# Kernel tuning notes

Hardware: AMD Instinct MI355X
Metric: run time of the kernel (lower is better)

## Reference

```python
import jax, jax.numpy as jnp
import numpy as np

# DeformConv (v1, mmcv-style) config
N, C, H, W = 4, 64, 128, 128
OUT_C, KH, KW = 64, 3, 3
STRIDE, PAD, DIL, DG = 1, 1, 1, 1  # groups = 1


def setup_inputs() -> dict:
    key = jax.random.key(0)
    k1, k2, k3 = jax.random.split(key, 3)
    x = jax.random.normal(k1, (N, C, H, W), dtype=jnp.float32)
    offset = jax.random.normal(k2, (N, 2 * DG * KH * KW, H, W), dtype=jnp.float32)
    n_fan = C * KH * KW
    std = 1.0 / np.sqrt(n_fan)
    weight = jax.random.uniform(k3, (OUT_C, C, KH, KW), minval=-std, maxval=std, dtype=jnp.float32)
    return {"input_tensor": x, "offset": offset, "weight": weight}


def _deform_conv(x, offset, weight, stride, padding, dilation, dg):
    n, c, h, w = x.shape
    o, cin_g, kh, kw = weight.shape
    k = kh * kw
    ho = (h + 2 * padding - dilation * (kh - 1) - 1) // stride + 1
    wo = (w + 2 * padding - dilation * (kw - 1) - 1) // stride + 1

    # offset layout: [n, dg*k*2, ho, wo] with (dy, dx) pairs per kernel point
    off = offset.reshape(n, dg, k, 2, ho, wo)
    dy, dx = off[:, :, :, 0], off[:, :, :, 1]  # [n, dg, k, ho, wo]

    ky, kx = jnp.meshgrid(jnp.arange(kh), jnp.arange(kw), indexing="ij")
    ky = ky.reshape(k).astype(x.dtype)
    kx = kx.reshape(k).astype(x.dtype)

    base_y = (jnp.arange(ho) * stride - padding).astype(x.dtype)
    base_x = (jnp.arange(wo) * stride - padding).astype(x.dtype)
    # sampling positions [n, dg, k, ho, wo]
    py = base_y[None, None, None, :, None] + (ky * dilation)[None, None, :, None, None] + dy
    px = base_x[None, None, None, None, :] + (kx * dilation)[None, None, :, None, None] + dx

    cg = c // dg
    xg = x.reshape(n, dg, cg, h * w)

    y0 = jnp.floor(py)
    x0 = jnp.floor(px)
    ly = py - y0  # bilinear weights
    lx = px - x0
    y0i = y0.astype(jnp.int32)
    x0i = x0.astype(jnp.int32)

    def gather(yi, xi):
        # zero contribution for out-of-bounds neighbors (matches mmcv bilinear)
        valid = (yi >= 0) & (yi < h) & (xi >= 0) & (xi < w)
        idx = jnp.clip(yi, 0, h - 1) * w + jnp.clip(xi, 0, w - 1)  # [n, dg, k, ho, wo]
        v = jnp.take_along_axis(xg, idx.reshape(n, dg, 1, -1), axis=3)  # [n, dg, cg, k*ho*wo]
        v = v.reshape(n, dg, cg, k, ho, wo)
        return v * valid[:, :, None].astype(x.dtype)

    v00 = gather(y0i, x0i)
    v01 = gather(y0i, x0i + 1)
    v10 = gather(y0i + 1, x0i)
    v11 = gather(y0i + 1, x0i + 1)

    wy = ly[:, :, None]  # [n, dg, 1, k, ho, wo]
    wx = lx[:, :, None]
    sampled = (v00 * (1 - wy) * (1 - wx) + v01 * (1 - wy) * wx
               + v10 * wy * (1 - wx) + v11 * wy * wx)
    sampled = sampled.reshape(n, c, k, ho, wo)  # dg*cg == c, groups == 1

    return jnp.einsum("nckhw,ock->nohw", sampled, weight.reshape(o, cin_g, k))


def reference(input_tensor, offset, weight):
    return _deform_conv(input_tensor, offset, weight, STRIDE, PAD, DIL, DG)
```

## Files before the change

### kernel.cpp

```cpp
#include <hip/hip_runtime.h>

#define HW 16384
#define CIN 64
#define COUT 64
#define HH 128
#define WW 128
#define NB 4
#define PXB 16
#define TPB 8

typedef __attribute__((ext_vector_type(8))) short bf16x8;
typedef __attribute__((ext_vector_type(4))) float f32x4;
typedef __attribute__((ext_vector_type(4))) unsigned short u16x4;

__device__ __forceinline__ unsigned short f32_bf16(float f) {
  unsigned u = __builtin_bit_cast(unsigned, f);
  u += 0x7fffu + ((u >> 16) & 1u);
  return (unsigned short)(u >> 16);
}
__device__ __forceinline__ float bits_f32(unsigned u) {
  return __builtin_bit_cast(float, u);
}

#define SYNCB()                                              \
  do {                                                       \
    asm volatile("s_waitcnt lgkmcnt(0)" ::: "memory");       \
    __builtin_amdgcn_s_barrier();                            \
    __builtin_amdgcn_sched_barrier(0);                       \
  } while (0)

__global__ __launch_bounds__(256) void prep_kernel(
    const float* __restrict__ x, const float* __restrict__ w,
    unsigned short* __restrict__ xt, unsigned short* __restrict__ wt) {
  __shared__ float tile[64][65];
  const int bid = blockIdx.x;
  if (bid < 1024) {
    const int n = bid >> 8;
    const int hw0 = (bid & 255) * 64;
    const int tx = threadIdx.x & 63;
    const int ty = threadIdx.x >> 6;
    const float* xp = x + (size_t)n * CIN * HW;
    #pragma unroll
    for (int c = ty; c < 64; c += 4)
      tile[c][tx] = xp[(size_t)c * HW + hw0 + tx];
    __syncthreads();
    unsigned short* xtp = xt + (size_t)n * HW * CIN;
    #pragma unroll
    for (int hw = ty; hw < 64; hw += 4)
      xtp[(size_t)(hw0 + hw) * CIN + tx] = f32_bf16(tile[tx][hw]);
  } else {
    const int i = (bid - 1024) * 256 + threadIdx.x;
    if (i < 64 * 576) {
      const int o = i / 576;
      const int t = i % 576;
      const int c = t & 63;
      const int k = t >> 6;
      wt[i] = f32_bf16(w[((size_t)o * 64 + c) * 9 + k]);
    }
  }
}

__global__ __launch_bounds__(256, 2) void deform_mfma(
    const unsigned short* __restrict__ xt, const float* __restrict__ offset,
    const unsigned short* __restrict__ wt, float* __restrict__ out) {
  __shared__ unsigned short s[PXB][584];
  __shared__ f32x4 pw[2][144];
  __shared__ uint2 pidx[2][144];
  const int tid = threadIdx.x;
  const int wave = tid >> 6;
  const int lane = tid & 63;
  const int g = lane >> 4;
  const int li = lane & 15;
  const int base = blockIdx.x * (PXB * TPB);
  const int n = base >> 14;
  const int rem_base = base & 16383;

  const float* offb = offset + (size_t)n * 18 * HW;
  const unsigned short* xli = xt + (size_t)n * HW * CIN + li * 4;

  const int px0 = tid & 15;
  const int tap0 = tid >> 4;
  const bool pthr = tap0 < 9;
  const int px = wave * 4 + g;

  bf16x8 bv[18];
  {
    const unsigned short* bp = wt + ((size_t)(wave * 16 + li)) * 576 + g * 8;
    #pragma unroll
    for (int i = 0; i < 18; ++i)
      bv[i] = *(const bf16x8*)(bp + i * 32);
  }

  #define PARAMS(tt, wb)                                                   \
    do {                                                                   \
      const int rem = rem_base + (tt) * PXB + px0;                         \
      const int y = rem >> 7;                                              \
      const int x = rem & 127;                                             \
      const float fy = floorf(dy);                                         \
      const float fx = floorf(dx);                                         \
      const float ly = dy - fy;                                            \
      const float lx = dx - fx;                                            \
      const int y0 = y - 1 + (tap0 / 3) + (int)fy;                         \
      const int x0 = x - 1 + (tap0 % 3) + (int)fx;                         \
      const int y1 = y0 + 1, x1 = x0 + 1;                                  \
      const bool vy0 = (unsigned)y0 < (unsigned)HH;                        \
      const bool vy1 = (unsigned)y1 < (unsigned)HH;                        \
      const bool vx0 = (unsigned)x0 < (unsigned)WW;                        \
      const bool vx1 = (unsigned)x1 < (unsigned)WW;                        \
      const int cy0 = min(max(y0, 0), HH - 1);                             \
      const int cy1 = min(max(y1, 0), HH - 1);                             \
      const int cx0 = min(max(x0, 0), WW - 1);                             \
      const int cx1 = min(max(x1, 0), WW - 1);                             \
      const float omly = 1.f - ly, omlx = 1.f - lx;                        \
      f32x4 w4;                                                            \
      w4[0] = (vy0 && vx0) ? omly * omlx : 0.f;                            \
      w4[1] = (vy0 && vx1) ? omly * lx : 0.f;                              \
      w4[2] = (vy1 && vx0) ? ly * omlx : 0.f;                              \
      w4[3] = (vy1 && vx1) ? ly * lx : 0.f;                                \
      const unsigned i00 = (unsigned)(cy0 * WW + cx0);                     \
      const unsigned i01 = (unsigned)(cy0 * WW + cx1);                     \
      const unsigned i10 = (unsigned)(cy1 * WW + cx0);                     \
      const unsigned i11 = (unsigned)(cy1 * WW + cx1);                     \
      pw[wb][tid] = w4;                                                    \
      pidx[wb][tid] = make_uint2(i00 | (i01 << 16), i10 | (i11 << 16));    \
    } while (0)

  u16x4 V00[9], V01[9], V10[9], V11[9];

  #define GATHERS(rb)                                                      \
    do {                                                                   \
      uint2 id[9];                                                         \
      _Pragma("unroll")                                                    \
      for (int k = 0; k < 9; ++k) id[k] = pidx[rb][k * 16 + px];           \
      _Pragma("unroll")                                                    \
      for (int k = 0; k < 9; ++k) {                                        \
        V00[k] = *(const u16x4*)(xli + (size_t)(id[k].x & 0xffffu) * CIN); \
        V01[k] = *(const u16x4*)(xli + (size_t)(id[k].x >> 16) * CIN);     \
        V10[k] = *(const u16x4*)(xli + (size_t)(id[k].y & 0xffffu) * CIN); \
        V11[k] = *(const u16x4*)(xli + (size_t)(id[k].y >> 16) * CIN);     \
      }                                                                    \
      __builtin_amdgcn_sched_barrier(0);                                   \
    } while (0)

  #define MFMA_OUT(remt)                                                   \
    do {                                                                   \
      f32x4 acc0 = {0.f, 0.f, 0.f, 0.f};                                   \
      f32x4 acc1 = {0.f, 0.f, 0.f, 0.f};                                   \
      const unsigned short* ap = &s[li][g * 8];                            \
      _Pragma("unroll")                                                    \
      for (int i = 0; i < 18; i += 2) {                                    \
        bf16x8 av0 = *(const bf16x8*)(ap + i * 32);                        \
        bf16x8 av1 = *(const bf16x8*)(ap + (i + 1) * 32);                  \
        acc0 = __builtin_amdgcn_mfma_f32_16x16x32_bf16(av0, bv[i], acc0, 0, 0, 0); \
        acc1 = __builtin_amdgcn_mfma_f32_16x16x32_bf16(av1, bv[i + 1], acc1, 0, 0, 0); \
      }                                                                    \
      const f32x4 acc = acc0 + acc1;                                       \
      const int oc = wave * 16 + li;                                       \
      float* ob = out + ((size_t)n * COUT + oc) * HW + (remt) + g * 4;     \
      *(f32x4*)ob = acc;                                                   \
    } while (0)

  float dy = 0.f, dx = 0.f;
  if (pthr) {
    const int rem = rem_base + px0;
    dy = offb[(size_t)(2 * tap0) * HW + rem];
    dx = offb[(size_t)(2 * tap0 + 1) * HW + rem];
  }
  if (pthr) PARAMS(0, 0);
  if (pthr) {
    const int rem = rem_base + PXB + px0;
    dy = offb[(size_t)(2 * tap0) * HW + rem];
    dx = offb[(size_t)(2 * tap0 + 1) * HW + rem];
  }
  SYNCB();
  GATHERS(0);

  int prev_rem0 = 0;

  #pragma unroll 1
  for (int t = 0; t < TPB; ++t) {
    const int rem0 = rem_base + t * PXB;

    if (t > 0) MFMA_OUT(prev_rem0);

    if (t + 1 < TPB && pthr) PARAMS(t + 1, (t + 1) & 1);

    if (t + 2 < TPB && pthr) {
      const int rem = rem_base + (t + 2) * PXB + px0;
      dy = offb[(size_t)(2 * tap0) * HW + rem];
      dx = offb[(size_t)(2 * tap0 + 1) * HW + rem];
    }

    SYNCB();

    #pragma unroll
    for (int k = 0; k < 9; ++k) {
      const f32x4 w = pw[t & 1][k * 16 + px];
      float a0 = 0.f, a1 = 0.f, a2 = 0.f, a3 = 0.f;
      #define CORNER(v, wc)                                        \
        a0 = fmaf(bits_f32((unsigned)(v)[0] << 16), (wc), a0);     \
        a1 = fmaf(bits_f32((unsigned)(v)[1] << 16), (wc), a1);     \
        a2 = fmaf(bits_f32((unsigned)(v)[2] << 16), (wc), a2);     \
        a3 = fmaf(bits_f32((unsigned)(v)[3] << 16), (wc), a3);
      CORNER(V00[k], w[0]);
      CORNER(V01[k], w[1]);
      CORNER(V10[k], w[2]);
      CORNER(V11[k], w[3]);
      #undef CORNER
      unsigned r01, r23;
      asm("v_cvt_pk_bf16_f32 %0, %1, %2" : "=v"(r01) : "v"(a0), "v"(a1));
      asm("v_cvt_pk_bf16_f32 %0, %1, %2" : "=v"(r23) : "v"(a2), "v"(a3));
      *(uint2*)&s[px][k * 64 + li * 4] = make_uint2(r01, r23);
    }

    if (t + 1 < TPB) GATHERS((t + 1) & 1);

    SYNCB();
    prev_rem0 = rem0;
  }

  MFMA_OUT(prev_rem0);

  #undef PARAMS
  #undef GATHERS
  #undef MFMA_OUT
}

__global__ __launch_bounds__(256) void deform_fallback(
    const float* __restrict__ xsrc, const float* __restrict__ offset,
    const float* __restrict__ wsrc, float* __restrict__ out) {
  __shared__ float s[16][576];
  const int wave = threadIdx.x >> 6;
  const int lane = threadIdx.x & 63;
  const int p0 = blockIdx.x * 16;
  for (int i = 0; i < 4; ++i) {
    const int p = p0 + wave * 4 + i;
    const int n = p >> 14;
    const int rem = p & 16383;
    const int y = rem >> 7;
    const int x = rem & 127;
    const float* off = offset + (size_t)n * 18 * HW + rem;
    const float* xb = xsrc + (size_t)n * CIN * HW;
    #pragma unroll
    for (int k = 0; k < 9; ++k) {
      const float dy = off[(size_t)(2 * k) * HW];
      const float dx = off[(size_t)(2 * k + 1) * HW];
      const float py = (float)(y - 1 + k / 3) + dy;
      const float px = (float)(x - 1 + k % 3) + dx;
      const float y0f = floorf(py), x0f = floorf(px);
      const float ly = py - y0f, lx = px - x0f;
      const int y0 = (int)y0f, x0 = (int)x0f;
      const int y1 = y0 + 1, x1 = x0 + 1;
      const bool vy0 = (y0 >= 0) && (y0 < HH), vy1 = (y1 >= 0) && (y1 < HH);
      const bool vx0 = (x0 >= 0) && (x0 < WW), vx1 = (x1 >= 0) && (x1 < WW);
      const int cy0 = min(max(y0, 0), HH - 1), cy1 = min(max(y1, 0), HH - 1);
      const int cx0 = min(max(x0, 0), WW - 1), cx1 = min(max(x1, 0), WW - 1);
      const float v00 = (vy0 && vx0) ? xb[(size_t)lane * HW + cy0 * WW + cx0] : 0.f;
      const float v01 = (vy0 && vx1) ? xb[(size_t)lane * HW + cy0 * WW + cx1] : 0.f;
      const float v10 = (vy1 && vx0) ? xb[(size_t)lane * HW + cy1 * WW + cx0] : 0.f;
      const float v11 = (vy1 && vx1) ? xb[(size_t)lane * HW + cy1 * WW + cx1] : 0.f;
      s[wave * 4 + i][k * 64 + lane] =
          v00 * (1.f - ly) * (1.f - lx) + v01 * (1.f - ly) * lx +
          v10 * ly * (1.f - lx) + v11 * ly * lx;
    }
  }
  __syncthreads();
  float a0 = 0.f, a1 = 0.f, a2 = 0.f, a3 = 0.f;
  const int pb = wave * 4;
  for (int t = 0; t < 576; ++t) {
    const int c = t & 63;
    const int k = t >> 6;
    const float wv = wsrc[((size_t)lane * 64 + c) * 9 + k];
    a0 += s[pb + 0][t] * wv;
    a1 += s[pb + 1][t] * wv;
    a2 += s[pb + 2][t] * wv;
    a3 += s[pb + 3][t] * wv;
  }
  const float acc[4] = {a0, a1, a2, a3};
  for (int i = 0; i < 4; ++i) {
    const int p = p0 + pb + i;
    const int n = p >> 14;
    const int rem = p & 16383;
    out[((size_t)n * COUT + lane) * HW + rem] = acc[i];
  }
}

extern "C" void kernel_launch(void* const* d_in, const int* in_sizes, int n_in,
                              void* d_out, int out_size, void* d_ws,
                              size_t ws_size, hipStream_t stream) {
  const float* x = (const float*)d_in[0];
  const float* offset = (const float*)d_in[1];
  const float* weight = (const float*)d_in[2];
  float* out = (float*)d_out;

  const size_t xt_elems = (size_t)NB * HW * CIN;
  const size_t wt_elems = (size_t)64 * 576;
  const size_t need = (xt_elems + wt_elems) * sizeof(short);

  if (ws_size >= need) {
    unsigned short* xtp = (unsigned short*)d_ws;
    unsigned short* wtp = xtp + xt_elems;
    prep_kernel<<<1024 + 144, 256, 0, stream>>>(x, weight, xtp, wtp);
    deform_mfma<<<NB * HW / (PXB * TPB), 256, 0, stream>>>(xtp, offset, wtp, out);
  } else {
    deform_fallback<<<NB * HW / 16, 256, 0, stream>>>(x, offset, weight, out);
  }
}
```

Baseline: 43.93 us.

## Double pixel tile, widen gathers to 8 channels, rolling 3-slot gather pipeline

Each block iteration now covers 32 pixels instead of 16, and each lane gathers 8 bf16 channels per corner instead of 4. Corner values are held in a rolling three-slot register ring where blending tap k overlaps the loads for tap k+3. The full cross-tile double buffering of parameters and gathers is replaced by computing parameters at the start of each iteration, which removes the 36 u16x4 registers that held corner values across iterations. Each MFMA pass now issues two independent 16-pixel tiles against shared B fragments. The trade-off is less gather latency hidden across iterations, since each tile's gathers now start only after its own parameter sync.

```diff
diff --git a/kernel.cpp b/kernel.cpp
--- a/kernel.cpp
+++ b/kernel.cpp
@@ -6,12 +6,12 @@
 #define HH 128
 #define WW 128
 #define NB 4
-#define PXB 16
-#define TPB 8
+#define PXB 32
+#define TPB 4
 
 typedef __attribute__((ext_vector_type(8))) short bf16x8;
 typedef __attribute__((ext_vector_type(4))) float f32x4;
-typedef __attribute__((ext_vector_type(4))) unsigned short u16x4;
+typedef __attribute__((ext_vector_type(8))) unsigned short u16x8;
 
 __device__ __forceinline__ unsigned short f32_bf16(float f) {
   unsigned u = __builtin_bit_cast(unsigned, f);
@@ -64,44 +64,44 @@
     const unsigned short* __restrict__ xt, const float* __restrict__ offset,
     const unsigned short* __restrict__ wt, float* __restrict__ out) {
   __shared__ unsigned short s[PXB][584];
-  __shared__ f32x4 pw[2][144];
-  __shared__ uint2 pidx[2][144];
+  __shared__ f32x4 pw[288];
+  __shared__ uint2 pidx[288];
   const int tid = threadIdx.x;
   const int wave = tid >> 6;
   const int lane = tid & 63;
-  const int g = lane >> 4;
-  const int li = lane & 15;
+  const int g16 = lane >> 4;
+  const int li16 = lane & 15;
+  const int px = wave * 8 + (lane >> 3);
+  const int li8 = lane & 7;
   const int base = blockIdx.x * (PXB * TPB);
   const int n = base >> 14;
   const int rem_base = base & 16383;
 
   const float* offb = offset + (size_t)n * 18 * HW;
-  const unsigned short* xli = xt + (size_t)n * HW * CIN + li * 4;
-
-  const int px0 = tid & 15;
-  const int tap0 = tid >> 4;
-  const bool pthr = tap0 < 9;
-  const int px = wave * 4 + g;
+  const unsigned short* xli = xt + (size_t)n * HW * CIN + li8 * 8;
+
+  const int px0 = tid & 31;
+  const int tap0 = tid >> 5;
 
   bf16x8 bv[18];
   {
-    const unsigned short* bp = wt + ((size_t)(wave * 16 + li)) * 576 + g * 8;
+    const unsigned short* bp = wt + ((size_t)(wave * 16 + li16)) * 576 + g16 * 8;
     #pragma unroll
     for (int i = 0; i < 18; ++i)
       bv[i] = *(const bf16x8*)(bp + i * 32);
   }
 
-  #define PARAMS(tt, wb)                                                   \
+  #define PARAMS(tt, tapv, dyv, dxv)                                       \
     do {                                                                   \
       const int rem = rem_base + (tt) * PXB + px0;                         \
       const int y = rem >> 7;                                              \
       const int x = rem & 127;                                             \
-      const float fy = floorf(dy);                                         \
-      const float fx = floorf(dx);                                         \
-      const float ly = dy - fy;                                            \
-      const float lx = dx - fx;                                            \
-      const int y0 = y - 1 + (tap0 / 3) + (int)fy;                         \
-      const int x0 = x - 1 + (tap0 % 3) + (int)fx;                         \
+      const float fy = floorf(dyv);                                        \
+      const float fx = floorf(dxv);                                        \
+      const float ly = (dyv)-fy;                                           \
+      const float lx = (dxv)-fx;                                           \
+      const int y0 = y - 1 + ((tapv) / 3) + (int)fy;                       \
+      const int x0 = x - 1 + ((tapv) % 3) + (int)fx;                       \
       const int y1 = y0 + 1, x1 = x0 + 1;                                  \
       const bool vy0 = (unsigned)y0 < (unsigned)HH;                        \
       const bool vy1 = (unsigned)y1 < (unsigned)HH;                        \
@@ -121,59 +121,68 @@
       const unsigned i01 = (unsigned)(cy0 * WW + cx1);                     \
       const unsigned i10 = (unsigned)(cy1 * WW + cx0);                     \
       const unsigned i11 = (unsigned)(cy1 * WW + cx1);                     \
-      pw[wb][tid] = w4;                                                    \
-      pidx[wb][tid] = make_uint2(i00 | (i01 << 16), i10 | (i11 << 16));    \
+      pw[(tapv)*32 + px0] = w4;                                            \
+      pidx[(tapv)*32 + px0] = make_uint2(i00 | (i01 << 16), i10 | (i11 << 16)); \
     } while (0)
 
-  u16x4 V00[9], V01[9], V10[9], V11[9];
-
-  #define GATHERS(rb)                                                      \
+  u16x8 V[3][4];
+
+  #define ISSUE(kk, sl)                                                    \
     do {                                                                   \
-      uint2 id[9];                                                         \
+      const uint2 id = pidx[(kk)*32 + px];                                 \
+      V[sl][0] = *(const u16x8*)(xli + (size_t)(id.x & 0xffffu) * CIN);    \
+      V[sl][1] = *(const u16x8*)(xli + (size_t)(id.x >> 16) * CIN);        \
+      V[sl][2] = *(const u16x8*)(xli + (size_t)(id.y & 0xffffu) * CIN);    \
+      V[sl][3] = *(const u16x8*)(xli + (size_t)(id.y >> 16) * CIN);        \
+    } while (0)
+
+  #define BLEND(kk, sl)                                                    \
+    do {                                                                   \
+      const f32x4 w = pw[(kk)*32 + px];                                    \
+      float a[8] = {0.f, 0.f, 0.f, 0.f, 0.f, 0.f, 0.f, 0.f};               \
       _Pragma("unroll")                                                    \
-      for (int k = 0; k < 9; ++k) id[k] = pidx[rb][k * 16 + px];           \
-      _Pragma("unroll")                                                    \
-      for (int k = 0; k < 9; ++k) {                                        \
-        V00[k] = *(const u16x4*)(xli + (size_t)(id[k].x & 0xffffu) * CIN); \
-        V01[k] = *(const u16x4*)(xli + (size_t)(id[k].x >> 16) * CIN);     \
-        V10[k] = *(const u16x4*)(xli + (size_t)(id[k].y & 0xffffu) * CIN); \
-        V11[k] = *(const u16x4*)(xli + (size_t)(id[k].y >> 16) * CIN);     \
+      for (int c = 0; c < 4; ++c) {                                        \
+        _Pragma("unroll")                                                  \
+        for (int j = 0; j < 8; ++j)                                        \
+          a[j] = fmaf(bits_f32((unsigned)V[sl][c][j] << 16), w[c], a[j]);  \
       }                                                                    \
-      __builtin_amdgcn_sched_barrier(0);                                   \
+      unsigned r0, r1, r2, r3;                                             \
+      asm("v_cvt_pk_bf16_f32 %0, %1, %2" : "=v"(r0) : "v"(a[0]), "v"(a[1])); \
+      asm("v_cvt_pk_bf16_f32 %0, %1, %2" : "=v"(r1) : "v"(a[2]), "v"(a[3])); \
+      asm("v_cvt_pk_bf16_f32 %0, %1, %2" : "=v"(r2) : "v"(a[4]), "v"(a[5])); \
+      asm("v_cvt_pk_bf16_f32 %0, %1, %2" : "=v"(r3) : "v"(a[6]), "v"(a[7])); \
+      *(uint4*)&s[px][(kk)*64 + li8 * 8] = make_uint4(r0, r1, r2, r3);     \
     } while (0)
 
   #define MFMA_OUT(remt)                                                   \
     do {                                                                   \
       f32x4 acc0 = {0.f, 0.f, 0.f, 0.f};                                   \
       f32x4 acc1 = {0.f, 0.f, 0.f, 0.f};                                   \
-      const unsigned short* ap = &s[li][g * 8];                            \
+      const unsigned short* ap0 = &s[li16][g16 * 8];                       \
+      const unsigned short* ap1 = &s[16 + li16][g16 * 8];                  \
       _Pragma("unroll")                                                    \
-      for (int i = 0; i < 18; i += 2) {                                    \
-        bf16x8 av0 = *(const bf16x8*)(ap + i * 32);                        \
-        bf16x8 av1 = *(const bf16x8*)(ap + (i + 1) * 32);                  \
-        acc0 = __builtin_amdgcn_mfma_f32_16x16x32_bf16(av0, bv[i], acc0, 0, 0, 0); \
-        acc1 = __builtin_amdgcn_mfma_f32_16x16x32_bf16(av1, bv[i + 1], acc1, 0, 0, 0); \
+      for (int i = 0; i < 18; ++i) {                                       \
+        bf16x8 a0 = *(const bf16x8*)(ap0 + i * 32);                        \
+        bf16x8 a1 = *(const bf16x8*)(ap1 + i * 32);                        \
+        acc0 = __builtin_amdgcn_mfma_f32_16x16x32_bf16(a0, bv[i], acc0, 0, 0, 0); \
+        acc1 = __builtin_amdgcn_mfma_f32_16x16x32_bf16(a1, bv[i], acc1, 0, 0, 0); \
       }                                                                    \
-      const f32x4 acc = acc0 + acc1;                                       \
-      const int oc = wave * 16 + li;                                       \
-      float* ob = out + ((size_t)n * COUT + oc) * HW + (remt) + g * 4;     \
-      *(f32x4*)ob = acc;                                                   \
+      const int oc = wave * 16 + li16;                                     \
+      float* ob = out + ((size_t)n * COUT + oc) * HW + (remt) + g16 * 4;   \
+      *(f32x4*)ob = acc0;                                                  \
+      *(f32x4*)(ob + 16) = acc1;                                           \
     } while (0)
 
-  float dy = 0.f, dx = 0.f;
-  if (pthr) {
+  float dy0, dx0, dy1 = 0.f, dx1 = 0.f;
+  {
     const int rem = rem_base + px0;
-    dy = offb[(size_t)(2 * tap0) * HW + rem];
-    dx = offb[(size_t)(2 * tap0 + 1) * HW + rem];
-  }
-  if (pthr) PARAMS(0, 0);
-  if (pthr) {
-    const int rem = rem_base + PXB + px0;
-    dy = offb[(size_t)(2 * tap0) * HW + rem];
-    dx = offb[(size_t)(2 * tap0 + 1) * HW + rem];
-  }
-  SYNCB();
-  GATHERS(0);
+    dy0 = offb[(size_t)(2 * tap0) * HW + rem];
+    dx0 = offb[(size_t)(2 * tap0 + 1) * HW + rem];
+    if (tid < 32) {
+      dy1 = offb[(size_t)16 * HW + rem];
+      dx1 = offb[(size_t)17 * HW + rem];
+    }
+  }
 
   int prev_rem0 = 0;
 
@@ -181,48 +190,47 @@
   for (int t = 0; t < TPB; ++t) {
     const int rem0 = rem_base + t * PXB;
 
+    PARAMS(t, tap0, dy0, dx0);
+    if (tid < 32) PARAMS(t, 8, dy1, dx1);
+    SYNCB();
+
+    if (t + 1 < TPB) {
+      const int rem = rem_base + (t + 1) * PXB + px0;
+      dy0 = offb[(size_t)(2 * tap0) * HW + rem];
+      dx0 = offb[(size_t)(2 * tap0 + 1) * HW + rem];
+      if (tid < 32) {
+        dy1 = offb[(size_t)16 * HW + rem];
+        dx1 = offb[(size_t)17 * HW + rem];
+      }
+    }
+
+    ISSUE(0, 0);
+    ISSUE(1, 1);
+    ISSUE(2, 2);
+    __builtin_amdgcn_sched_barrier(0);
+
     if (t > 0) MFMA_OUT(prev_rem0);
-
-    if (t + 1 < TPB && pthr) PARAMS(t + 1, (t + 1) & 1);
-
-    if (t + 2 < TPB && pthr) {
-      const int rem = rem_base + (t + 2) * PXB + px0;
-      dy = offb[(size_t)(2 * tap0) * HW + rem];
-      dx = offb[(size_t)(2 * tap0 + 1) * HW + rem];
-    }
-
     SYNCB();
 
-    #pragma unroll
-    for (int k = 0; k < 9; ++k) {
-      const f32x4 w = pw[t & 1][k * 16 + px];
-      float a0 = 0.f, a1 = 0.f, a2 = 0.f, a3 = 0.f;
-      #define CORNER(v, wc)                                        \
-        a0 = fmaf(bits_f32((unsigned)(v)[0] << 16), (wc), a0);     \
-        a1 = fmaf(bits_f32((unsigned)(v)[1] << 16), (wc), a1);     \
-        a2 = fmaf(bits_f32((unsigned)(v)[2] << 16), (wc), a2);     \
-        a3 = fmaf(bits_f32((unsigned)(v)[3] << 16), (wc), a3);
-      CORNER(V00[k], w[0]);
-      CORNER(V01[k], w[1]);
-      CORNER(V10[k], w[2]);
-      CORNER(V11[k], w[3]);
-      #undef CORNER
-      unsigned r01, r23;
-      asm("v_cvt_pk_bf16_f32 %0, %1, %2" : "=v"(r01) : "v"(a0), "v"(a1));
-      asm("v_cvt_pk_bf16_f32 %0, %1, %2" : "=v"(r23) : "v"(a2), "v"(a3));
-      *(uint2*)&s[px][k * 64 + li * 4] = make_uint2(r01, r23);
-    }
-
-    if (t + 1 < TPB) GATHERS((t + 1) & 1);
-
+    BLEND(0, 0); ISSUE(3, 0);
+    BLEND(1, 1); ISSUE(4, 1);
+    BLEND(2, 2); ISSUE(5, 2);
+    BLEND(3, 0); ISSUE(6, 0);
+    BLEND(4, 1); ISSUE(7, 1);
+    BLEND(5, 2); ISSUE(8, 2);
+    BLEND(6, 0);
+    BLEND(7, 1);
+    BLEND(8, 2);
     SYNCB();
+
     prev_rem0 = rem0;
   }
 
   MFMA_OUT(prev_rem0);
 
   #undef PARAMS
-  #undef GATHERS
+  #undef ISSUE
+  #undef BLEND
   #undef MFMA_OUT
 }
 
```

Result: faster. 36.27 us (-17.4%).
